# Kernel tuning notes

Hardware: AMD Instinct MI355X
Metric: run time of the kernel (lower is better)

The kernel has to match this reference:

```python
import jax, jax.numpy as jnp
import numpy as np

EPS = 1e-6      # eps used in token2map / map2token weight normalization
LN_EPS = 1e-5   # torch nn.LayerNorm default


def layernorm(x, w, b):
    m = jnp.mean(x, axis=-1, keepdims=True)
    xc = x - m
    v = jnp.mean(xc * xc, axis=-1, keepdims=True)
    return xc * jax.lax.rsqrt(v + LN_EPS) * w + b


def grid_index(H_init, W_init, H, W):
    # nearest-neighbor map: flattened feature-map index for each init-grid cell
    r = (jnp.arange(H_init) * H) // H_init
    c = (jnp.arange(W_init) * W) // W_init
    return (r[:, None] * W + c[None, :]).reshape(-1)  # [N_init]


def token2map(x, idx_token, H, W, H_init, W_init):
    # tokens [B,N,C] -> feature map [B,H,W,C] via weighted scatter-mean
    B, N, C = x.shape
    idx_hw = grid_index(H_init, W_init, H, W)                    # [N_init]
    counts = jnp.zeros((H * W,), x.dtype).at[idx_hw].add(1.0)    # identical across batch
    w = (1.0 / (counts + EPS))[idx_hw]                           # [N_init]
    src = jnp.take_along_axis(x, idx_token[..., None], axis=1)   # [B,N_init,C]
    out = jnp.zeros((B, H * W, C), x.dtype).at[:, idx_hw, :].add(src * w[None, :, None])
    return out.reshape(B, H, W, C)


def map2token(fmap, idx_token, N, H_init, W_init):
    # feature map [B,H,W,C] -> tokens [B,N,C]: mean of member grid cells per token
    B, H, W, C = fmap.shape
    idx_hw = grid_index(H_init, W_init, H, W)
    bidx = jnp.arange(B)[:, None]
    counts = jnp.zeros((B, N), fmap.dtype).at[bidx, idx_token].add(1.0)
    wt = jnp.take_along_axis(1.0 / (counts + EPS), idx_token, axis=1)  # [B,N_init]
    src = fmap.reshape(B, H * W, C)[:, idx_hw, :]                      # [B,N_init,C]
    return jnp.zeros((B, N, C), fmap.dtype).at[bidx, idx_token].add(src * wt[..., None])


def _forward(x, token_score, idx_token,
             norm1_w, norm1_b, q_w, q_b, kv_w, kv_b, sr_w, sr_b, srn_w, srn_b,
             proj_w, proj_b, norm2_w, norm2_b, fc1_w, fc1_b, skip_w, dw_w, dw_b,
             fc2_w, fc2_b, H, W, H_init, W_init, token_num, num_heads):
    B, N, C = x.shape
    d = C // num_heads
    scale = d ** -0.5
    sr = 2  # sr_ratio

    xn = layernorm(x, norm1_w, norm1_b)  # q_dict['x'] = norm1(x); kv_dict is q_dict

    # ---- TCFormerDynamicAttention ----
    q = (xn @ q_w + q_b).reshape(B, N, num_heads, d).transpose(0, 2, 1, 3)  # [B,h,N,d]
    tmp = jnp.concatenate([xn, token_score], axis=-1)            # [B,N,C+1]
    tmp_map = token2map(tmp, idx_token, H, W, H_init, W_init)    # [B,H,W,C+1]
    kv_map, conf_map = tmp_map[..., :C], tmp_map[..., C]
    kv = jax.lax.conv_general_dilated(kv_map, sr_w, (sr, sr), 'VALID',
        dimension_numbers=('NHWC', 'HWIO', 'NHWC')) + sr_b       # sr conv, stride 2
    M = (H // sr) * (W // sr)
    kv = layernorm(kv.reshape(B, M, C), srn_w, srn_b)
    conf = conf_map.reshape(B, H // sr, sr, W // sr, sr).mean(axis=(2, 4)).reshape(B, M)

    kv = (kv @ kv_w + kv_b).reshape(B, M, 2, num_heads, d)
    k = kv[:, :, 0].transpose(0, 2, 1, 3)                        # [B,h,M,d]
    v = kv[:, :, 1].transpose(0, 2, 1, 3)
    attn = jnp.einsum('bhnd,bhmd->bhnm', q * scale, k) + conf[:, None, None, :]
    attn = jax.nn.softmax(attn, axis=-1)
    a = jnp.einsum('bhnm,bhmd->bhnd', attn, v).transpose(0, 2, 1, 3).reshape(B, N, C)
    x = x + (a @ proj_w + proj_b)

    # ---- TCMLP ----
    h = layernorm(x, norm2_w, norm2_b) @ fc1_w + fc1_b           # [B,N,H1]
    hmap = token2map(h, idx_token, H, W, H_init, W_init)         # [B,H,W,H1]
    hmap = jax.lax.conv_general_dilated(hmap, dw_w, (1, 1), ((1, 1), (1, 1)),
        dimension_numbers=('NHWC', 'HWIO', 'NHWC'),
        feature_group_count=h.shape[-1]) + dw_b                  # depthwise 3x3
    hc = h * skip_w + map2token(hmap, idx_token, N, H_init, W_init)  # skip = dw 1x1 conv1d
    hc = jax.nn.gelu(hc, approximate=False)
    return x + (hc @ fc2_w + fc2_b)


def setup_inputs() -> dict:
    B, N, C, H1 = 8, 1568, 256, 1024
    H = W = 56
    H_init = W_init = 112
    key = jax.random.key(0)
    ks = jax.random.split(key, 16)
    r = lambda i, shape, s=0.02: jax.random.normal(ks[i], shape, jnp.float32) * s
    return {
        'x': jax.random.normal(ks[0], (B, N, C), jnp.float32),
        'token_score': jax.random.normal(ks[1], (B, N, 1), jnp.float32),
        'idx_token': jax.random.randint(ks[2], (B, H_init * W_init), 0, N),
        'norm1_w': jnp.ones((C,), jnp.float32), 'norm1_b': jnp.zeros((C,), jnp.float32),
        'q_w': r(3, (C, C)), 'q_b': jnp.zeros((C,), jnp.float32),
        'kv_w': r(4, (C, 2 * C)), 'kv_b': jnp.zeros((2 * C,), jnp.float32),
        'sr_w': r(5, (2, 2, C, C)), 'sr_b': jnp.zeros((C,), jnp.float32),
        'srn_w': jnp.ones((C,), jnp.float32), 'srn_b': jnp.zeros((C,), jnp.float32),
        'proj_w': r(6, (C, C)), 'proj_b': jnp.zeros((C,), jnp.float32),
        'norm2_w': jnp.ones((C,), jnp.float32), 'norm2_b': jnp.zeros((C,), jnp.float32),
        'fc1_w': r(7, (C, H1)), 'fc1_b': jnp.zeros((H1,), jnp.float32),
        'skip_w': 1.0 + r(8, (H1,), 0.1),
        'dw_w': r(9, (3, 3, 1, H1), 0.1), 'dw_b': jnp.zeros((H1,), jnp.float32),
        'fc2_w': r(10, (H1, C)), 'fc2_b': jnp.zeros((C,), jnp.float32),
        'H': H, 'W': W, 'H_init': H_init, 'W_init': W_init,
        'token_num': N, 'num_heads': 8,
    }


def reference(x, token_score, idx_token, norm1_w, norm1_b, q_w, q_b, kv_w, kv_b,
              sr_w, sr_b, srn_w, srn_b, proj_w, proj_b, norm2_w, norm2_b,
              fc1_w, fc1_b, skip_w, dw_w, dw_b, fc2_w, fc2_b,
              H, W, H_init, W_init, token_num, num_heads):
    return _forward(x, token_score, idx_token, norm1_w, norm1_b, q_w, q_b, kv_w, kv_b,
                    sr_w, sr_b, srn_w, srn_b, proj_w, proj_b, norm2_w, norm2_b,
                    fc1_w, fc1_b, skip_w, dw_w, dw_b, fc2_w, fc2_b,
                    H, W, H_init, W_init, token_num, num_heads)
```

## Files before the change

### kernel.cpp

```cpp
#include <hip/hip_runtime.h>
#include <math.h>

#define BB 8
#define NTOK 1568
#define CD 256
#define HIMG 56
#define WIMG 56
#define HWSZ 3136
#define HIG 112
#define WIG 112
#define NI 12544
#define MKV 784
#define MPAD 800
#define NHEADS 8
#define HEADD 32
#define HH1 1024
#define ROWS1 (BB*NTOK)
#define ROWSK (BB*MKV)
#define LOG2E 1.4426950408889634f

typedef unsigned short bfu;
typedef __attribute__((ext_vector_type(4))) unsigned short bf4;
typedef __attribute__((ext_vector_type(8))) unsigned short bf8;
typedef __attribute__((ext_vector_type(8))) short s8v;
typedef __attribute__((ext_vector_type(4))) float f4v;
typedef __attribute__((ext_vector_type(16))) float f16v;

__device__ inline float b2f(bfu u) { union { unsigned i; float f; } x; x.i = (unsigned)u << 16; return x.f; }
__device__ inline bfu f2b(float f) {
  union { float f; unsigned i; } x; x.f = f;
  unsigned r = x.i + 0x7fffu + ((x.i >> 16) & 1u);
  return (bfu)(r >> 16);
}
__device__ inline int get_isb(const unsigned* probe) { return probe[0] == 0x3F803F80u ? 1 : 0; }
__device__ inline float ldd(const void* p, size_t i, int isb) {
  return isb ? b2f(((const bfu*)p)[i]) : ((const float*)p)[i];
}
__device__ inline int xswz(int wg, int nwg) {
  return (nwg & 7) ? wg : (wg & 7) * (nwg >> 3) + (wg >> 3);
}

__global__ __launch_bounds__(256) void wtr_tile(const void* __restrict__ w0,
                                                const void* __restrict__ w1,
                                                const void* __restrict__ w2,
                                                const void* __restrict__ w3,
                                                const void* __restrict__ w4,
                                                const void* __restrict__ w5,
                                                const void* __restrict__ w6,
                                                const void* __restrict__ w7,
                                                bfu* __restrict__ wtb,
                                                bfu* __restrict__ vt,
                                                float* __restrict__ conf,
                                                const unsigned* __restrict__ probe) {
  int isb = get_isb(probe);
  int bid = blockIdx.x, tid = threadIdx.x;
  if (bid >= 1064) {
    int t = (bid - 1064) * 256 + tid;
    int b = t / 4096, rem = t % 4096;
    int d = rem / 16, m = MKV + (rem % 16);
    vt[((size_t)(b * 256 + d)) * MPAD + m] = 0;
    if (t < 128) conf[(t / 16) * MPAD + MKV + (t % 16)] = -1e30f;
    return;
  }
  if (bid >= 1024) {
    int idx = (bid - 1024) * 256 + tid;
    if (idx < 9216) wtb[1048576 + idx] = f2b(ldd(w6, idx, isb));
    else            wtb[1048576 + idx] = f2b(ldd(w7, idx - 9216, isb));
    return;
  }
  const void* W; int K, N; bfu* Wt; int tloc;
  if (bid < 64)       { W = w0; K = 256;  N = 256;  Wt = wtb;          tloc = bid; }
  else if (bid < 320) { W = w1; K = 1024; N = 256;  Wt = wtb + 65536;  tloc = bid - 64; }
  else if (bid < 448) { W = w2; K = 256;  N = 512;  Wt = wtb + 327680; tloc = bid - 320; }
  else if (bid < 512) { W = w3; K = 256;  N = 256;  Wt = wtb + 458752; tloc = bid - 448; }
  else if (bid < 768) { W = w4; K = 256;  N = 1024; Wt = wtb + 524288; tloc = bid - 512; }
  else                { W = w5; K = 1024; N = 256;  Wt = wtb + 786432; tloc = bid - 768; }
  int ntn = N >> 5;
  int tn = tloc % ntn, tk = tloc / ntn;
  int n0 = tn * 32, k0 = tk * 32;
  __shared__ float s[32][33];
  int tx = tid & 31, ty = tid >> 5;
#pragma unroll
  for (int i = 0; i < 4; i++) {
    int k = ty + 8 * i;
    s[k][tx] = ldd(W, (size_t)(k0 + k) * N + n0 + tx, isb);
  }
  __syncthreads();
#pragma unroll
  for (int i = 0; i < 4; i++) {
    int n = ty + 8 * i;
    Wt[(size_t)(n0 + n) * K + k0 + tx] = f2b(s[tx][n]);
  }
}

__global__ __launch_bounds__(256) void ln_kernel(const void* __restrict__ in, int inmode,
                                                 const void* __restrict__ w,
                                                 const void* __restrict__ bta,
                                                 bfu* __restrict__ out,
                                                 const unsigned* __restrict__ probe) {
  int isb = get_isb(probe);
  int im = (inmode == 2) ? isb : inmode;
  int blk = xswz(blockIdx.x, gridDim.x);
  int wv = threadIdx.x >> 6, lane = threadIdx.x & 63;
  int row = blk * 4 + wv;
  int c4 = lane * 4;
  float v[4];
  if (im) {
    bf4 t = *(const bf4*)((const bfu*)in + (size_t)row * CD + c4);
#pragma unroll
    for (int j = 0; j < 4; j++) v[j] = b2f(t[j]);
  } else {
    float4 t = *(const float4*)((const float*)in + (size_t)row * CD + c4);
    v[0] = t.x; v[1] = t.y; v[2] = t.z; v[3] = t.w;
  }
  float s1 = v[0] + v[1] + v[2] + v[3];
  float s2 = v[0] * v[0] + v[1] * v[1] + v[2] * v[2] + v[3] * v[3];
#pragma unroll
  for (int off = 1; off < 64; off <<= 1) {
    s1 += __shfl_xor(s1, off);
    s2 += __shfl_xor(s2, off);
  }
  float m = s1 * (1.0f / CD);
  float inv = rsqrtf(s2 * (1.0f / CD) - m * m + 1e-5f);
  bf4 ov;
#pragma unroll
  for (int j = 0; j < 4; j++)
    ov[j] = f2b((v[j] - m) * inv * ldd(w, c4 + j, isb) + ldd(bta, c4 + j, isb));
  *(bf4*)(out + (size_t)row * CD + c4) = ov;
}

__device__ inline void gemm2ph_body(int id,
                                    const bfu* __restrict__ A,
                                    const bfu* __restrict__ Bt,
                                    const void* __restrict__ bias,
                                    const void* __restrict__ resid, int rm,
                                    void* __restrict__ Cc, int cm,
                                    void* __restrict__ aux,
                                    int K, int Ncols, int isb) {
  __shared__ bfu As[2][64][40];
  __shared__ bfu Bs[2][64][40];
  int t = threadIdx.x;
  int nbx = Ncols >> 6;
  int row0 = (id / nbx) * 64, col0 = (id % nbx) * 64;
  int sr = t >> 2, sc = (t & 3) * 8;
  int w = t >> 6, lane = t & 63;
  int li = lane & 15, q = lane >> 4;
  int wm = w * 16;
  const bfu* pa = A + (size_t)(row0 + sr) * K + sc;
  const bfu* pb = Bt + (size_t)(col0 + sr) * K + sc;
  f4v zz = {0.f, 0.f, 0.f, 0.f};
  f4v acc[4];
#pragma unroll
  for (int ni = 0; ni < 4; ni++) acc[ni] = zz;
  s8v la = *(const s8v*)(pa);
  s8v lb = *(const s8v*)(pb);
  int cur = 0;
  for (int k0 = 32; k0 <= K; k0 += 32) {
    *(s8v*)(&As[cur][sr][sc]) = la;
    *(s8v*)(&Bs[cur][sr][sc]) = lb;
    __syncthreads();
    if (k0 < K) {
      la = *(const s8v*)(pa + k0);
      lb = *(const s8v*)(pb + k0);
    }
    s8v af  = *(const s8v*)(&As[cur][wm + li][q * 8]);
    s8v bf0 = *(const s8v*)(&Bs[cur][li][q * 8]);
    s8v bf1 = *(const s8v*)(&Bs[cur][16 + li][q * 8]);
    s8v bf2 = *(const s8v*)(&Bs[cur][32 + li][q * 8]);
    s8v bf3 = *(const s8v*)(&Bs[cur][48 + li][q * 8]);
    __builtin_amdgcn_s_setprio(1);
    acc[0] = __builtin_amdgcn_mfma_f32_16x16x32_bf16(af, bf0, acc[0], 0, 0, 0);
    acc[1] = __builtin_amdgcn_mfma_f32_16x16x32_bf16(af, bf1, acc[1], 0, 0, 0);
    acc[2] = __builtin_amdgcn_mfma_f32_16x16x32_bf16(af, bf2, acc[2], 0, 0, 0);
    acc[3] = __builtin_amdgcn_mfma_f32_16x16x32_bf16(af, bf3, acc[3], 0, 0, 0);
    __builtin_amdgcn_s_setprio(0);
    cur ^= 1;
  }
  float bw[4];
#pragma unroll
  for (int ni = 0; ni < 4; ni++) bw[ni] = ldd(bias, col0 + ni * 16 + li, isb);
#pragma unroll
  for (int ni = 0; ni < 4; ni++) {
    int col = col0 + ni * 16 + li;
#pragma unroll
    for (int r = 0; r < 4; r++) {
      int row = row0 + wm + q * 4 + r;
      size_t base = (size_t)row * Ncols + col;
      float v = acc[ni][r] + bw[ni];
      if (rm == 2) v += ((const float*)resid)[base];
      else if (rm == 3) v += b2f(((const bfu*)resid)[base]);
      if (cm == 0) ((bfu*)Cc)[base] = f2b(v);
      else if (cm == 1) ((float*)Cc)[base] = v;
      else {
        if (col < 256) ((bfu*)Cc)[base] = f2b(v);
        else {
          int bb = row / MKV, mm = row - bb * MKV;
          ((bfu*)aux)[((size_t)(bb * 256) + (col - 256)) * MPAD + mm] = f2b(v);
        }
      }
    }
  }
}

__global__ __launch_bounds__(256) void gemm2ph(const bfu* __restrict__ A,
                                               const bfu* __restrict__ Bt,
                                               const void* __restrict__ bias,
                                               const void* __restrict__ resid, int rmode,
                                               void* __restrict__ Cc, int cmode,
                                               void* __restrict__ aux,
                                               int K, int Ncols,
                                               const unsigned* __restrict__ probe) {
  int isb = get_isb(probe);
  int rm = (rmode == 1) ? (isb ? 3 : 2) : rmode;
  int cm = (cmode == 2) ? (isb ? 0 : 1) : cmode;
  gemm2ph_body(xswz(blockIdx.x, gridDim.x), A, Bt, bias, resid, rm, Cc, cm, aux, K, Ncols, isb);
}

__device__ inline void akv_body(int blk,
                                const bfu* __restrict__ xn,
                                const void* __restrict__ tscore,
                                const int* __restrict__ idx_token,
                                bfu* __restrict__ Akv,
                                float* __restrict__ conf, int isb) {
  int tid = threadIdx.x;
  int b = blk / MKV, m = blk % MKV;
  int i2 = m / 28, j2 = m % 28;
  __shared__ int nn[16];
  __shared__ float cacc[16];
  if (tid < 16) {
    int a = (tid >> 3) & 1, kb = (tid >> 2) & 1, di = (tid >> 1) & 1, dj = tid & 1;
    int ti = 4 * i2 + 2 * a + di, tj = 4 * j2 + 2 * kb + dj;
    int n = idx_token[b * NI + ti * WIG + tj];
    nn[tid] = n;
    cacc[tid] = ldd(tscore, b * NTOK + n, isb);
  }
  __syncthreads();
  const float w4 = 1.0f / (4.0f + 1e-6f);
  int g = tid >> 6, c4 = (tid & 63) * 4;
  bf4 a0 = *(const bf4*)(xn + (size_t)(b * NTOK + nn[g * 4 + 0]) * CD + c4);
  bf4 a1 = *(const bf4*)(xn + (size_t)(b * NTOK + nn[g * 4 + 1]) * CD + c4);
  bf4 a2 = *(const bf4*)(xn + (size_t)(b * NTOK + nn[g * 4 + 2]) * CD + c4);
  bf4 a3 = *(const bf4*)(xn + (size_t)(b * NTOK + nn[g * 4 + 3]) * CD + c4);
  bf4 rv;
#pragma unroll
  for (int j = 0; j < 4; j++)
    rv[j] = f2b(w4 * (b2f(a0[j]) + b2f(a1[j]) + b2f(a2[j]) + b2f(a3[j])));
  *(bf4*)(Akv + (size_t)blk * 1024 + g * CD + c4) = rv;
  if (tid == 0) {
    float s = 0.f;
    for (int k = 0; k < 16; k++) s += cacc[k];
    conf[b * MPAD + m] = 0.25f * w4 * s * 5.656854249492381f;
  }
}

__global__ __launch_bounds__(256) void qakv_kernel(const bfu* __restrict__ xn,
                                                   const bfu* __restrict__ q_wt,
                                                   const void* __restrict__ q_b,
                                                   bfu* __restrict__ qbuf,
                                                   const void* __restrict__ tscore,
                                                   const int* __restrict__ idx_token,
                                                   bfu* __restrict__ Akv,
                                                   float* __restrict__ conf,
                                                   const unsigned* __restrict__ probe) {
  int isb = get_isb(probe);
  if (blockIdx.x < 784)
    gemm2ph_body(xswz(blockIdx.x, 784), xn, q_wt, q_b, nullptr, 0, qbuf, 0, nullptr, 256, 256, isb);
  else
    akv_body(xswz(blockIdx.x - 784, 6272), xn, tscore, idx_token, Akv, conf, isb);
}

__global__ __launch_bounds__(256) void attn_kernel(const bfu* __restrict__ qb,
                                                   const bfu* __restrict__ kv,
                                                   const bfu* __restrict__ vt,
                                                   const float* __restrict__ conf,
                                                   bfu* __restrict__ out) {
  __shared__ float sdata[4][64][17];
  int tid = threadIdx.x;
  int w = tid >> 6, lane = tid & 63;
  int l31 = lane & 31, hi = lane >> 5;
  int blk = xswz(blockIdx.x, gridDim.x);
  int qt = blk % 25, tt = blk / 25;
  int hh = tt & 7, b = tt >> 3;
  int n0 = qt * 64;
  int two = (qt < 24);
  const bfu* qrow1 = qb + (size_t)(b * NTOK + n0 + l31) * CD + hh * HEADD + hi * 8;
  s8v qfA1 = *(const s8v*)(qrow1);
  s8v qfB1 = *(const s8v*)(qrow1 + 16);
  s8v qfA2 = {0, 0, 0, 0, 0, 0, 0, 0}, qfB2 = qfA2;
  if (two) {
    const bfu* qrow2 = qrow1 + (size_t)32 * CD;
    qfA2 = *(const s8v*)(qrow2);
    qfB2 = *(const s8v*)(qrow2 + 16);
  }
  const float scale = 0.17677669529663689f * LOG2E;
  const bfu* kbase = kv + hh * HEADD + hi * 8;
  const bfu* vbase = vt + ((size_t)(b * 256 + hh * HEADD + l31)) * MPAD + hi * 8;
  const float* cbase = conf + b * MPAD + 4 * hi;
  f16v oc1, oc2;
#pragma unroll
  for (int r = 0; r < 16; r++) { oc1[r] = 0.f; oc2[r] = 0.f; }
  float lr1 = 0.f, lr2 = 0.f;
  int w32 = w * 32;
  const bfu* kp0 = kbase + (size_t)(b * MKV + w32 + l31) * 512;
  s8v kfA = *(const s8v*)(kp0);
  s8v kfB = *(const s8v*)(kp0 + 16);
  s8v vfA = *(const s8v*)(vbase + w32);
  s8v vfB = *(const s8v*)(vbase + w32 + 16);
  float4 cf0 = *(const float4*)(cbase + w32);
  float4 cf1 = *(const float4*)(cbase + w32 + 8);
  float4 cf2 = *(const float4*)(cbase + w32 + 16);
  float4 cf3 = *(const float4*)(cbase + w32 + 24);
  for (int m0 = w32; m0 < MPAD; m0 += 128) {
    s8v ckA = kfA, ckB = kfB, cvA = vfA, cvB = vfB;
    float4 d0 = cf0, d1 = cf1, d2 = cf2, d3 = cf3;
    int m1 = m0 + 128;
    if (m1 < MPAD) {
      int mA = m1 + l31; if (mA > MKV - 1) mA = MKV - 1;
      const bfu* kp = kbase + (size_t)(b * MKV + mA) * 512;
      kfA = *(const s8v*)(kp);
      kfB = *(const s8v*)(kp + 16);
      vfA = *(const s8v*)(vbase + m1);
      vfB = *(const s8v*)(vbase + m1 + 16);
      cf0 = *(const float4*)(cbase + m1);
      cf1 = *(const float4*)(cbase + m1 + 8);
      cf2 = *(const float4*)(cbase + m1 + 16);
      cf3 = *(const float4*)(cbase + m1 + 24);
    }
    f16v cseed;
    cseed[0] = d0.x; cseed[1] = d0.y; cseed[2] = d0.z; cseed[3] = d0.w;
    cseed[4] = d1.x; cseed[5] = d1.y; cseed[6] = d1.z; cseed[7] = d1.w;
    cseed[8] = d2.x; cseed[9] = d2.y; cseed[10] = d2.z; cseed[11] = d2.w;
    cseed[12] = d3.x; cseed[13] = d3.y; cseed[14] = d3.z; cseed[15] = d3.w;
    __builtin_amdgcn_s_setprio(1);
    f16v c = __builtin_amdgcn_mfma_f32_32x32x16_bf16(ckA, qfA1, cseed, 0, 0, 0);
    c = __builtin_amdgcn_mfma_f32_32x32x16_bf16(ckB, qfB1, c, 0, 0, 0);
    __builtin_amdgcn_s_setprio(0);
    {
      float p[16], ps0 = 0.f, ps1 = 0.f, ps2 = 0.f, ps3 = 0.f;
#pragma unroll
      for (int r = 0; r < 16; r++) {
        p[r] = __builtin_amdgcn_exp2f(c[r] * scale);
        if ((r & 3) == 0) ps0 += p[r];
        else if ((r & 3) == 1) ps1 += p[r];
        else if ((r & 3) == 2) ps2 += p[r];
        else ps3 += p[r];
      }
      lr1 += (ps0 + ps1) + (ps2 + ps3);
      unsigned Z[8];
#pragma unroll
      for (int a2 = 0; a2 < 8; a2++)
        asm("v_cvt_pk_bf16_f32 %0, %1, %2" : "=v"(Z[a2]) : "v"(p[2 * a2]), "v"(p[2 * a2 + 1]));
      asm("v_permlane32_swap_b32 %0, %1" : "+v"(Z[0]), "+v"(Z[2]));
      asm("v_permlane32_swap_b32 %0, %1" : "+v"(Z[1]), "+v"(Z[3]));
      asm("v_permlane32_swap_b32 %0, %1" : "+v"(Z[4]), "+v"(Z[6]));
      asm("v_permlane32_swap_b32 %0, %1" : "+v"(Z[5]), "+v"(Z[7]));
      union { unsigned u[4]; s8v v; } B1, B2;
      B1.u[0] = Z[0]; B1.u[1] = Z[1]; B1.u[2] = Z[2]; B1.u[3] = Z[3];
      B2.u[0] = Z[4]; B2.u[1] = Z[5]; B2.u[2] = Z[6]; B2.u[3] = Z[7];
      __builtin_amdgcn_s_setprio(1);
      oc1 = __builtin_amdgcn_mfma_f32_32x32x16_bf16(cvA, B1.v, oc1, 0, 0, 0);
      oc1 = __builtin_amdgcn_mfma_f32_32x32x16_bf16(cvB, B2.v, oc1, 0, 0, 0);
      __builtin_amdgcn_s_setprio(0);
    }
    if (two) {
      __builtin_amdgcn_s_setprio(1);
      f16v c2 = __builtin_amdgcn_mfma_f32_32x32x16_bf16(ckA, qfA2, cseed, 0, 0, 0);
      c2 = __builtin_amdgcn_mfma_f32_32x32x16_bf16(ckB, qfB2, c2, 0, 0, 0);
      __builtin_amdgcn_s_setprio(0);
      float p[16], ps0 = 0.f, ps1 = 0.f, ps2 = 0.f, ps3 = 0.f;
#pragma unroll
      for (int r = 0; r < 16; r++) {
        p[r] = __builtin_amdgcn_exp2f(c2[r] * scale);
        if ((r & 3) == 0) ps0 += p[r];
        else if ((r & 3) == 1) ps1 += p[r];
        else if ((r & 3) == 2) ps2 += p[r];
        else ps3 += p[r];
      }
      lr2 += (ps0 + ps1) + (ps2 + ps3);
      unsigned Z[8];
#pragma unroll
      for (int a2 = 0; a2 < 8; a2++)
        asm("v_cvt_pk_bf16_f32 %0, %1, %2" : "=v"(Z[a2]) : "v"(p[2 * a2]), "v"(p[2 * a2 + 1]));
      asm("v_permlane32_swap_b32 %0, %1" : "+v"(Z[0]), "+v"(Z[2]));
      asm("v_permlane32_swap_b32 %0, %1" : "+v"(Z[1]), "+v"(Z[3]));
      asm("v_permlane32_swap_b32 %0, %1" : "+v"(Z[4]), "+v"(Z[6]));
      asm("v_permlane32_swap_b32 %0, %1" : "+v"(Z[5]), "+v"(Z[7]));
      union { unsigned u[4]; s8v v; } B1, B2;
      B1.u[0] = Z[0]; B1.u[1] = Z[1]; B1.u[2] = Z[2]; B1.u[3] = Z[3];
      B2.u[0] = Z[4]; B2.u[1] = Z[5]; B2.u[2] = Z[6]; B2.u[3] = Z[7];
      __builtin_amdgcn_s_setprio(1);
      oc2 = __builtin_amdgcn_mfma_f32_32x32x16_bf16(cvA, B1.v, oc2, 0, 0, 0);
      oc2 = __builtin_amdgcn_mfma_f32_32x32x16_bf16(cvB, B2.v, oc2, 0, 0, 0);
      __builtin_amdgcn_s_setprio(0);
    }
  }
#pragma unroll
  for (int r = 0; r < 16; r++) sdata[w][lane][r] = oc1[r];
  sdata[w][lane][16] = lr1;
  __syncthreads();
  if (w == 0) {
    float s[17];
#pragma unroll
    for (int r = 0; r < 17; r++)
      s[r] = sdata[0][lane][r] + sdata[1][lane][r] + sdata[2][lane][r] + sdata[3][lane][r];
    float l = s[16];
    l += __shfl_xor(l, 32);
    float inv = 1.0f / l;
    bfu* op = out + (size_t)(b * NTOK + n0 + l31) * CD + hh * HEADD + 4 * hi;
#pragma unroll
    for (int g = 0; g < 4; g++) {
      bf4 o;
#pragma unroll
      for (int u = 0; u < 4; u++) o[u] = f2b(s[4 * g + u] * inv);
      *(bf4*)(op + 8 * g) = o;
    }
  }
  if (two) {
    __syncthreads();
#pragma unroll
    for (int r = 0; r < 16; r++) sdata[w][lane][r] = oc2[r];
    sdata[w][lane][16] = lr2;
    __syncthreads();
    if (w == 0) {
      float s[17];
#pragma unroll
      for (int r = 0; r < 17; r++)
        s[r] = sdata[0][lane][r] + sdata[1][lane][r] + sdata[2][lane][r] + sdata[3][lane][r];
      float l = s[16];
      l += __shfl_xor(l, 32);
      float inv = 1.0f / l;
      bfu* op = out + (size_t)(b * NTOK + n0 + 32 + l31) * CD + hh * HEADD + 4 * hi;
#pragma unroll
      for (int g = 0; g < 4; g++) {
        bf4 o;
#pragma unroll
        for (int u = 0; u < 4; u++) o[u] = f2b(s[4 * g + u] * inv);
        *(bf4*)(op + 8 * g) = o;
      }
    }
  }
}

__device__ inline void hmap_body(int blk, const bfu* __restrict__ h,
                                 const int* __restrict__ idx_token,
                                 bfu* __restrict__ hmap) {
  int tid = threadIdx.x;
  int b = blk / HWSZ, cell = blk % HWSZ;
  int i = cell / WIMG, j = cell % WIMG;
  __shared__ int nn[4];
  if (tid < 4) {
    int di = tid >> 1, dj = tid & 1;
    nn[tid] = idx_token[b * NI + (2 * i + di) * WIG + (2 * j + dj)];
  }
  __syncthreads();
  const float w4 = 1.0f / (4.0f + 1e-6f);
  int c8 = tid * 8;
  bf8 a0 = *(const bf8*)(h + (size_t)(b * NTOK + nn[0]) * HH1 + c8);
  bf8 a1 = *(const bf8*)(h + (size_t)(b * NTOK + nn[1]) * HH1 + c8);
  bf8 a2 = *(const bf8*)(h + (size_t)(b * NTOK + nn[2]) * HH1 + c8);
  bf8 a3 = *(const bf8*)(h + (size_t)(b * NTOK + nn[3]) * HH1 + c8);
  bf8 rv;
#pragma unroll
  for (int j2 = 0; j2 < 8; j2++)
    rv[j2] = f2b(w4 * (b2f(a0[j2]) + b2f(a1[j2]) + b2f(a2[j2]) + b2f(a3[j2])));
  *(bf8*)(hmap + (size_t)blk * HH1 + c8) = rv;
}

__global__ __launch_bounds__(128) void hmapcnt_kernel(const bfu* __restrict__ h,
                                                      const int* __restrict__ idx_token,
                                                      bfu* __restrict__ hmap,
                                                      int* __restrict__ cnt) {
  if (blockIdx.x < 25088) {
    hmap_body(xswz(blockIdx.x, 25088), h, idx_token, hmap);
  } else {
    int t = xswz(blockIdx.x - 25088, 784) * 128 + threadIdx.x;
    int b = t / NI;
    atomicAdd(&cnt[b * NTOK + idx_token[t]], 1);
  }
}

__device__ inline void dw_body(int blk, const bfu* __restrict__ hmap,
                               const bfu* __restrict__ dwt,
                               const bfu* __restrict__ dbt,
                               bfu* __restrict__ dwout) {
  int j8 = blk % 7; int rem = blk / 7;
  int i = rem % HIMG; int b = rem / HIMG;
  int tid = threadIdx.x;
  int c4 = tid * 4;
  int j0 = j8 * 8;
  float wf[9][4];
#pragma unroll
  for (int k = 0; k < 9; k++) {
    bf4 wv = *(const bf4*)(dwt + k * HH1 + c4);
#pragma unroll
    for (int u = 0; u < 4; u++) wf[k][u] = b2f(wv[u]);
  }
  bf4 bias = *(const bf4*)(dbt + c4);
  float bi[4];
#pragma unroll
  for (int u = 0; u < 4; u++) bi[u] = b2f(bias[u]);
  bf4 tp[3][10];
  const size_t bbase = (size_t)b * HWSZ;
#pragma unroll
  for (int r = 0; r < 3; r++) {
    int yy = i - 1 + r;
    bool rowok = (unsigned)yy < (unsigned)HIMG;
#pragma unroll
    for (int cc = 0; cc < 10; cc++) {
      int xx = j0 - 1 + cc;
      bf4 v = {0, 0, 0, 0};
      if (rowok && (unsigned)xx < (unsigned)WIMG)
        v = *(const bf4*)(hmap + (bbase + yy * WIMG + xx) * HH1 + c4);
      tp[r][cc] = v;
    }
  }
#pragma unroll
  for (int j = 0; j < 8; j++) {
    float acc[4] = {bi[0], bi[1], bi[2], bi[3]};
#pragma unroll
    for (int r = 0; r < 3; r++)
#pragma unroll
      for (int kx = 0; kx < 3; kx++) {
        bf4 hv = tp[r][j + kx];
#pragma unroll
        for (int u = 0; u < 4; u++) acc[u] += b2f(hv[u]) * wf[r * 3 + kx][u];
      }
    bf4 ov;
#pragma unroll
    for (int u = 0; u < 4; u++) ov[u] = f2b(acc[u]);
    *(bf4*)(dwout + (bbase + i * WIMG + j0 + j) * HH1 + c4) = ov;
  }
}

__device__ inline void scan_body(int b, const int* __restrict__ cnt, int2* __restrict__ co) {
  int tid = threadIdx.x;
  __shared__ int s[NTOK];
  for (int i = tid; i < NTOK; i += 256) s[i] = cnt[b * NTOK + i];
  __syncthreads();
  for (int st = 1; st < NTOK; st <<= 1) {
    int vals[7]; int k = 0;
    for (int i = tid; i < NTOK; i += 256, k++) vals[k] = (i >= st) ? s[i - st] : 0;
    __syncthreads();
    k = 0;
    for (int i = tid; i < NTOK; i += 256, k++) s[i] += vals[k];
    __syncthreads();
  }
  for (int i = tid; i < NTOK; i += 256) {
    int2 v; v.x = cnt[b * NTOK + i]; v.y = (i > 0) ? s[i - 1] : 0;
    co[b * NTOK + i] = v;
  }
}

__global__ __launch_bounds__(256) void dwscan_kernel(const bfu* __restrict__ hmap,
                                                     const bfu* __restrict__ dwt,
                                                     const bfu* __restrict__ dbt,
                                                     bfu* __restrict__ dwout,
                                                     const int* __restrict__ cnt,
                                                     int2* __restrict__ co) {
  if (blockIdx.x < 3136) dw_body(xswz(blockIdx.x, 3136), hmap, dwt, dbt, dwout);
  else scan_body(blockIdx.x - 3136, cnt, co);
}

__global__ void fill_kernel(const int* __restrict__ idx, const int2* __restrict__ co,
                            int* __restrict__ cursor, int* __restrict__ tlist) {
  int t = xswz(blockIdx.x, gridDim.x) * 256 + threadIdx.x;
  int b = t / NI, tt = t % NI;
  int n = idx[t];
  int p = atomicAdd(&cursor[b * NTOK + n], 1);
  tlist[b * NI + co[b * NTOK + n].y + p] = tt;
}

__global__ __launch_bounds__(128) void m2t_kernel(const bfu* __restrict__ h,
                                                  const bfu* __restrict__ dwout,
                                                  const int2* __restrict__ co,
                                                  const int* __restrict__ tlist,
                                                  const void* __restrict__ skipw,
                                                  bfu* __restrict__ hc,
                                                  const unsigned* __restrict__ probe) {
  int isb = get_isb(probe);
  int blk = xswz(blockIdx.x, gridDim.x), tid = threadIdx.x;
  int lane = tid & 63;
  int row0 = blk * 2;
  int b = row0 / NTOK;
  int c8 = tid * 8;
  bf8 hv0 = *(const bf8*)(h + (size_t)row0 * HH1 + c8);
  bf8 hv1 = *(const bf8*)(h + (size_t)(row0 + 1) * HH1 + c8);
  int4 cc = *(const int4*)(co + row0);
  int cA = cc.x, oA = cc.y, cB = cc.z, oB = cc.w;
  float invA = 1.0f / ((float)cA + 1e-6f);
  float invB = 1.0f / ((float)cB + 1e-6f);
  float a0[8] = {}, a1[8] = {};
  int cmax = cA > cB ? cA : cB;
  for (int k0 = 0; k0 < cmax; k0 += 8) {
    int kk = k0 + (lane & 7);
    int eA = 0, eB = 0;
    if (kk < cA) eA = tlist[b * NI + oA + kk];
    if (kk < cB) eB = tlist[b * NI + oB + kk];
#pragma unroll
    for (int j = 0; j < 8; j++) {
      if (k0 + j < cA) {
        int tt = __shfl(eA, j);
        int ti = tt / WIG, tj = tt % WIG;
        int cell = (ti >> 1) * WIMG + (tj >> 1);
        bf8 dv = *(const bf8*)(dwout + ((size_t)b * HWSZ + cell) * HH1 + c8);
#pragma unroll
        for (int j2 = 0; j2 < 8; j2++) a0[j2] += b2f(dv[j2]);
      }
      if (k0 + j < cB) {
        int tt = __shfl(eB, j);
        int ti = tt / WIG, tj = tt % WIG;
        int cell = (ti >> 1) * WIMG + (tj >> 1);
        bf8 dv = *(const bf8*)(dwout + ((size_t)b * HWSZ + cell) * HH1 + c8);
#pragma unroll
        for (int j2 = 0; j2 < 8; j2++) a1[j2] += b2f(dv[j2]);
      }
    }
  }
  const float is2 = 0.70710678118654752f;
  bf8 ov0, ov1;
#pragma unroll
  for (int j2 = 0; j2 < 8; j2++) {
    float sw = ldd(skipw, c8 + j2, isb);
    float r0 = b2f(hv0[j2]) * sw + a0[j2] * invA;
    r0 = 0.5f * r0 * (1.0f + erff(r0 * is2));
    ov0[j2] = f2b(r0);
    float r1 = b2f(hv1[j2]) * sw + a1[j2] * invB;
    r1 = 0.5f * r1 * (1.0f + erff(r1 * is2));
    ov1[j2] = f2b(r1);
  }
  *(bf8*)(hc + (size_t)row0 * HH1 + c8) = ov0;
  *(bf8*)(hc + (size_t)(row0 + 1) * HH1 + c8) = ov1;
}

extern "C" void kernel_launch(void* const* d_in, const int* in_sizes, int n_in,
                              void* d_out, int out_size, void* d_ws, size_t ws_size,
                              hipStream_t stream) {
  const void* x        = d_in[0];
  const void* tscore   = d_in[1];
  const int*  idx_tok  = (const int*)d_in[2];
  const void* norm1_w  = d_in[3];
  const void* norm1_b  = d_in[4];
  const void* q_w      = d_in[5];
  const void* q_b      = d_in[6];
  const void* kv_w     = d_in[7];
  const void* kv_b     = d_in[8];
  const void* sr_w     = d_in[9];
  const void* sr_b     = d_in[10];
  const void* srn_w    = d_in[11];
  const void* srn_b    = d_in[12];
  const void* proj_w   = d_in[13];
  const void* proj_b   = d_in[14];
  const void* norm2_w  = d_in[15];
  const void* norm2_b  = d_in[16];
  const void* fc1_w    = d_in[17];
  const void* fc1_b    = d_in[18];
  const void* skip_w   = d_in[19];
  const void* dw_w     = d_in[20];
  const void* dw_b     = d_in[21];
  const void* fc2_w    = d_in[22];
  const void* fc2_b    = d_in[23];
  const unsigned* probe = (const unsigned*)d_in[3];

  float* ws = (float*)d_ws;
  size_t o = 0;
  float* x2 = ws + o;          o += (size_t)ROWS1 * CD;
  float* hR = ws + o;          o += (size_t)ROWS1 * HH1 / 2;
  float* mR = ws + o;          o += (size_t)BB * HWSZ * HH1 / 2;
  float* dR = ws + o;          o += (size_t)BB * HWSZ * HH1 / 2;
  int* ibase = (int*)(ws + o); o += (size_t)(4 * ROWS1 + BB * NI);
  bfu* wtb   = (bfu*)(ws + o); o += 529408;
  bfu* vtb   = (bfu*)(ws + o);

  bfu* Akv   = (bfu*)hR;
  bfu* kvc   = (bfu*)(hR + (size_t)ROWSK * 1024 / 2);
  bfu* h     = (bfu*)hR;
  bfu* qbuf  = (bfu*)mR;
  bfu* kvout = (bfu*)(mR + (size_t)ROWS1 * CD / 2);
  float* conf  = mR + (size_t)ROWS1 * CD / 2 + (size_t)ROWSK * 512 / 2;
  bfu* hmap  = (bfu*)mR;
  bfu* hc    = (bfu*)mR;
  bfu* xn    = (bfu*)dR;
  bfu* dwout = (bfu*)dR;
  int* counts = ibase;
  int* cursor = ibase + ROWS1;
  int2* co2   = (int2*)(ibase + 2 * ROWS1);
  int* tlist  = ibase + 4 * ROWS1;
  bfu* q_wt    = wtb;
  bfu* sr_wt   = wtb + 65536;
  bfu* kv_wt   = wtb + 327680;
  bfu* proj_wt = wtb + 458752;
  bfu* fc1_wt  = wtb + 524288;
  bfu* fc2_wt  = wtb + 786432;
  bfu* dwt     = wtb + 1048576;
  bfu* dbt     = wtb + 1057792;

  wtr_tile<<<1192, 256, 0, stream>>>(q_w, sr_w, kv_w, proj_w, fc1_w, fc2_w, dw_w, dw_b,
                                     wtb, vtb, conf, probe);
  hipMemsetAsync(counts, 0, (size_t)(2 * ROWS1) * sizeof(int), stream);

  ln_kernel<<<ROWS1 / 4, 256, 0, stream>>>(x, 2, norm1_w, norm1_b, xn, probe);
  qakv_kernel<<<7056, 256, 0, stream>>>(xn, q_wt, q_b, qbuf, tscore, idx_tok, Akv, conf, probe);
  gemm2ph<<<392, 256, 0, stream>>>(Akv, sr_wt, sr_b, nullptr, 0, kvc, 0, nullptr, 1024, 256, probe);
  ln_kernel<<<ROWSK / 4, 256, 0, stream>>>(kvc, 1, srn_w, srn_b, kvc, probe);
  gemm2ph<<<784, 256, 0, stream>>>(kvc, kv_wt, kv_b, nullptr, 0, kvout, 3, vtb, 256, 512, probe);
  attn_kernel<<<BB * NHEADS * 25, 256, 0, stream>>>(qbuf, kvout, vtb, conf, xn);
  gemm2ph<<<784, 256, 0, stream>>>(xn, proj_wt, proj_b, x, 1, x2, 1, nullptr, 256, 256, probe);
  ln_kernel<<<ROWS1 / 4, 256, 0, stream>>>(x2, 0, norm2_w, norm2_b, xn, probe);
  gemm2ph<<<3136, 256, 0, stream>>>(xn, fc1_wt, fc1_b, nullptr, 0, h, 0, nullptr, 256, 1024, probe);
  hmapcnt_kernel<<<25872, 128, 0, stream>>>(h, idx_tok, hmap, counts);
  dwscan_kernel<<<3144, 256, 0, stream>>>(hmap, dwt, dbt, dwout, counts, co2);
  fill_kernel<<<(BB * NI) / 256, 256, 0, stream>>>(idx_tok, co2, cursor, tlist);
  m2t_kernel<<<ROWS1 / 2, 128, 0, stream>>>(h, dwout, co2, tlist, skip_w, hc, probe);
  gemm2ph<<<784, 256, 0, stream>>>(hc, fc2_wt, fc2_b, x2, 2, d_out, 2, nullptr, 1024, 256, probe);
}
```

Before: 390.9 us.

## Enlarge GEMM tile to 128x64 and switch to 32x32x16 MFMA

The shared GEMM body now computes 128x64 output tiles instead of 64x64. Each wave owns 32 rows and uses two 32x32x16 bf16 MFMA accumulators in place of four 16x16x32 ones. All GEMM launch grids are halved to match. This aims to raise arithmetic intensity, so each B tile and LDS load is reused across twice as many rows. The cost is fewer workgroups, roughly 196 to 392 for most GEMMs on a device with many CUs, plus more registers. The epilogue now writes 32-wide column strips per lane group.

Measured after the change: 386.8 us. Within noise of the previous version (-1.0%).

```diff
diff --git a/kernel.cpp b/kernel.cpp
--- a/kernel.cpp
+++ b/kernel.cpp
@@ -23,7 +23,6 @@
 typedef __attribute__((ext_vector_type(4))) unsigned short bf4;
 typedef __attribute__((ext_vector_type(8))) unsigned short bf8;
 typedef __attribute__((ext_vector_type(8))) short s8v;
-typedef __attribute__((ext_vector_type(4))) float f4v;
 typedef __attribute__((ext_vector_type(16))) float f16v;
 
 __device__ inline float b2f(bfu u) { union { unsigned i; float f; } x; x.i = (unsigned)u << 16; return x.f; }
@@ -137,67 +136,70 @@
                                     void* __restrict__ Cc, int cm,
                                     void* __restrict__ aux,
                                     int K, int Ncols, int isb) {
-  __shared__ bfu As[2][64][40];
+  __shared__ bfu As[2][128][40];
   __shared__ bfu Bs[2][64][40];
   int t = threadIdx.x;
   int nbx = Ncols >> 6;
-  int row0 = (id / nbx) * 64, col0 = (id % nbx) * 64;
+  int row0 = (id / nbx) * 128, col0 = (id % nbx) * 64;
   int sr = t >> 2, sc = (t & 3) * 8;
   int w = t >> 6, lane = t & 63;
-  int li = lane & 15, q = lane >> 4;
-  int wm = w * 16;
-  const bfu* pa = A + (size_t)(row0 + sr) * K + sc;
-  const bfu* pb = Bt + (size_t)(col0 + sr) * K + sc;
-  f4v zz = {0.f, 0.f, 0.f, 0.f};
-  f4v acc[4];
-#pragma unroll
-  for (int ni = 0; ni < 4; ni++) acc[ni] = zz;
-  s8v la = *(const s8v*)(pa);
-  s8v lb = *(const s8v*)(pb);
+  int l31 = lane & 31, hi = lane >> 5;
+  int wm = w * 32;
+  const bfu* pa0 = A + (size_t)(row0 + sr) * K + sc;
+  const bfu* pa1 = pa0 + (size_t)64 * K;
+  const bfu* pb  = Bt + (size_t)(col0 + sr) * K + sc;
+  f16v acc0, acc1;
+#pragma unroll
+  for (int r = 0; r < 16; r++) { acc0[r] = 0.f; acc1[r] = 0.f; }
+  s8v la0 = *(const s8v*)(pa0);
+  s8v la1 = *(const s8v*)(pa1);
+  s8v lb  = *(const s8v*)(pb);
   int cur = 0;
   for (int k0 = 32; k0 <= K; k0 += 32) {
-    *(s8v*)(&As[cur][sr][sc]) = la;
+    *(s8v*)(&As[cur][sr][sc]) = la0;
+    *(s8v*)(&As[cur][sr + 64][sc]) = la1;
     *(s8v*)(&Bs[cur][sr][sc]) = lb;
     __syncthreads();
     if (k0 < K) {
-      la = *(const s8v*)(pa + k0);
-      lb = *(const s8v*)(pb + k0);
-    }
-    s8v af  = *(const s8v*)(&As[cur][wm + li][q * 8]);
-    s8v bf0 = *(const s8v*)(&Bs[cur][li][q * 8]);
-    s8v bf1 = *(const s8v*)(&Bs[cur][16 + li][q * 8]);
-    s8v bf2 = *(const s8v*)(&Bs[cur][32 + li][q * 8]);
-    s8v bf3 = *(const s8v*)(&Bs[cur][48 + li][q * 8]);
+      la0 = *(const s8v*)(pa0 + k0);
+      la1 = *(const s8v*)(pa1 + k0);
+      lb  = *(const s8v*)(pb + k0);
+    }
+    s8v afA = *(const s8v*)(&As[cur][wm + l31][hi * 8]);
+    s8v afB = *(const s8v*)(&As[cur][wm + l31][16 + hi * 8]);
+    s8v b0A = *(const s8v*)(&Bs[cur][l31][hi * 8]);
+    s8v b0B = *(const s8v*)(&Bs[cur][l31][16 + hi * 8]);
+    s8v b1A = *(const s8v*)(&Bs[cur][32 + l31][hi * 8]);
+    s8v b1B = *(const s8v*)(&Bs[cur][32 + l31][16 + hi * 8]);
     __builtin_amdgcn_s_setprio(1);
-    acc[0] = __builtin_amdgcn_mfma_f32_16x16x32_bf16(af, bf0, acc[0], 0, 0, 0);
-    acc[1] = __builtin_amdgcn_mfma_f32_16x16x32_bf16(af, bf1, acc[1], 0, 0, 0);
-    acc[2] = __builtin_amdgcn_mfma_f32_16x16x32_bf16(af, bf2, acc[2], 0, 0, 0);
-    acc[3] = __builtin_amdgcn_mfma_f32_16x16x32_bf16(af, bf3, acc[3], 0, 0, 0);
+    acc0 = __builtin_amdgcn_mfma_f32_32x32x16_bf16(afA, b0A, acc0, 0, 0, 0);
+    acc1 = __builtin_amdgcn_mfma_f32_32x32x16_bf16(afA, b1A, acc1, 0, 0, 0);
+    acc0 = __builtin_amdgcn_mfma_f32_32x32x16_bf16(afB, b0B, acc0, 0, 0, 0);
+    acc1 = __builtin_amdgcn_mfma_f32_32x32x16_bf16(afB, b1B, acc1, 0, 0, 0);
     __builtin_amdgcn_s_setprio(0);
     cur ^= 1;
   }
-  float bw[4];
-#pragma unroll
-  for (int ni = 0; ni < 4; ni++) bw[ni] = ldd(bias, col0 + ni * 16 + li, isb);
-#pragma unroll
-  for (int ni = 0; ni < 4; ni++) {
-    int col = col0 + ni * 16 + li;
-#pragma unroll
-    for (int r = 0; r < 4; r++) {
-      int row = row0 + wm + q * 4 + r;
-      size_t base = (size_t)row * Ncols + col;
-      float v = acc[ni][r] + bw[ni];
-      if (rm == 2) v += ((const float*)resid)[base];
-      else if (rm == 3) v += b2f(((const bfu*)resid)[base]);
-      if (cm == 0) ((bfu*)Cc)[base] = f2b(v);
-      else if (cm == 1) ((float*)Cc)[base] = v;
-      else {
-        if (col < 256) ((bfu*)Cc)[base] = f2b(v);
-        else {
-          int bb = row / MKV, mm = row - bb * MKV;
-          ((bfu*)aux)[((size_t)(bb * 256) + (col - 256)) * MPAD + mm] = f2b(v);
-        }
-      }
+  float bw0 = ldd(bias, col0 + l31, isb);
+  float bw1 = ldd(bias, col0 + 32 + l31, isb);
+#pragma unroll
+  for (int r = 0; r < 16; r++) {
+    int row = row0 + wm + (r & 3) + 8 * (r >> 2) + 4 * hi;
+    size_t base0 = (size_t)row * Ncols + col0 + l31;
+    size_t base1 = base0 + 32;
+    float v0 = acc0[r] + bw0;
+    float v1 = acc1[r] + bw1;
+    if (rm == 2) { v0 += ((const float*)resid)[base0]; v1 += ((const float*)resid)[base1]; }
+    else if (rm == 3) { v0 += b2f(((const bfu*)resid)[base0]); v1 += b2f(((const bfu*)resid)[base1]); }
+    if (cm == 0) { ((bfu*)Cc)[base0] = f2b(v0); ((bfu*)Cc)[base1] = f2b(v1); }
+    else if (cm == 1) { ((float*)Cc)[base0] = v0; ((float*)Cc)[base1] = v1; }
+    else {
+      int bb = row / MKV, mm = row - bb * MKV;
+      int col0c = col0 + l31;
+      if (col0c < 256) ((bfu*)Cc)[base0] = f2b(v0);
+      else ((bfu*)aux)[((size_t)(bb * 256) + (col0c - 256)) * MPAD + mm] = f2b(v0);
+      int col1c = col0c + 32;
+      if (col1c < 256) ((bfu*)Cc)[base1] = f2b(v1);
+      else ((bfu*)aux)[((size_t)(bb * 256) + (col1c - 256)) * MPAD + mm] = f2b(v1);
     }
   }
 }
@@ -263,10 +265,10 @@
                                                    float* __restrict__ conf,
                                                    const unsigned* __restrict__ probe) {
   int isb = get_isb(probe);
-  if (blockIdx.x < 784)
-    gemm2ph_body(xswz(blockIdx.x, 784), xn, q_wt, q_b, nullptr, 0, qbuf, 0, nullptr, 256, 256, isb);
+  if (blockIdx.x < 392)
+    gemm2ph_body(xswz(blockIdx.x, 392), xn, q_wt, q_b, nullptr, 0, qbuf, 0, nullptr, 256, 256, isb);
   else
-    akv_body(xswz(blockIdx.x - 784, 6272), xn, tscore, idx_token, Akv, conf, isb);
+    akv_body(xswz(blockIdx.x - 392, 6272), xn, tscore, idx_token, Akv, conf, isb);
 }
 
 __global__ __launch_bounds__(256) void attn_kernel(const bfu* __restrict__ qb,
@@ -699,17 +701,17 @@
   hipMemsetAsync(counts, 0, (size_t)(2 * ROWS1) * sizeof(int), stream);
 
   ln_kernel<<<ROWS1 / 4, 256, 0, stream>>>(x, 2, norm1_w, norm1_b, xn, probe);
-  qakv_kernel<<<7056, 256, 0, stream>>>(xn, q_wt, q_b, qbuf, tscore, idx_tok, Akv, conf, probe);
-  gemm2ph<<<392, 256, 0, stream>>>(Akv, sr_wt, sr_b, nullptr, 0, kvc, 0, nullptr, 1024, 256, probe);
+  qakv_kernel<<<6664, 256, 0, stream>>>(xn, q_wt, q_b, qbuf, tscore, idx_tok, Akv, conf, probe);
+  gemm2ph<<<196, 256, 0, stream>>>(Akv, sr_wt, sr_b, nullptr, 0, kvc, 0, nullptr, 1024, 256, probe);
   ln_kernel<<<ROWSK / 4, 256, 0, stream>>>(kvc, 1, srn_w, srn_b, kvc, probe);
-  gemm2ph<<<784, 256, 0, stream>>>(kvc, kv_wt, kv_b, nullptr, 0, kvout, 3, vtb, 256, 512, probe);
+  gemm2ph<<<392, 256, 0, stream>>>(kvc, kv_wt, kv_b, nullptr, 0, kvout, 3, vtb, 256, 512, probe);
   attn_kernel<<<BB * NHEADS * 25, 256, 0, stream>>>(qbuf, kvout, vtb, conf, xn);
-  gemm2ph<<<784, 256, 0, stream>>>(xn, proj_wt, proj_b, x, 1, x2, 1, nullptr, 256, 256, probe);
+  gemm2ph<<<392, 256, 0, stream>>>(xn, proj_wt, proj_b, x, 1, x2, 1, nullptr, 256, 256, probe);
   ln_kernel<<<ROWS1 / 4, 256, 0, stream>>>(x2, 0, norm2_w, norm2_b, xn, probe);
-  gemm2ph<<<3136, 256, 0, stream>>>(xn, fc1_wt, fc1_b, nullptr, 0, h, 0, nullptr, 256, 1024, probe);
+  gemm2ph<<<1568, 256, 0, stream>>>(xn, fc1_wt, fc1_b, nullptr, 0, h, 0, nullptr, 256, 1024, probe);
   hmapcnt_kernel<<<25872, 128, 0, stream>>>(h, idx_tok, hmap, counts);
   dwscan_kernel<<<3144, 256, 0, stream>>>(hmap, dwt, dbt, dwout, counts, co2);
   fill_kernel<<<(BB * NI) / 256, 256, 0, stream>>>(idx_tok, co2, cursor, tlist);
   m2t_kernel<<<ROWS1 / 2, 128, 0, stream>>>(h, dwout, co2, tlist, skip_w, hc, probe);
-  gemm2ph<<<784, 256, 0, stream>>>(hc, fc2_wt, fc2_b, x2, 2, d_out, 2, nullptr, 1024, 256, probe);
-}
+  gemm2ph<<<392, 256, 0, stream>>>(hc, fc2_wt, fc2_b, x2, 2, d_out, 2, nullptr, 1024, 256, probe);
+}
```
